# Kernel tuning notes

Hardware: AMD Instinct MI355X
Metric: run time of the kernel (lower is better)

Reference implementation:

```python
import jax, jax.numpy as jnp
import numpy as np

N_NODES = 100000
N_EDGES = 2000000
IN_X, IN_E, HID, OUT = 32, 64, 128, 64


def setup_inputs() -> dict:
    key = jax.random.key(0)
    ks = jax.random.split(key, 12)
    def w(k, shape, fan_in):
        return jax.random.normal(k, shape, dtype=jnp.float32) / np.sqrt(fan_in)
    x = jax.random.normal(ks[0], (N_NODES, IN_X), dtype=jnp.float32)
    edge_index = jax.random.randint(ks[1], (2, N_EDGES), 0, N_NODES)
    return {
        "x": x,
        "edge_index": edge_index,
        # initial_lin: in_x -> in_e
        "W0": w(ks[2], (IN_X, IN_E), IN_X),
        "b0": jnp.zeros((IN_E,), jnp.float32),
        # SAGEConv1: lin_l (aggregated neighbors, with bias), lin_r (self, no bias)
        "W1l": w(ks[3], (IN_E, HID), IN_E),
        "b1l": jnp.zeros((HID,), jnp.float32),
        "W1r": w(ks[4], (IN_E, HID), IN_E),
        # SAGEConv2
        "W2l": w(ks[5], (HID, OUT), HID),
        "b2l": jnp.zeros((OUT,), jnp.float32),
        "W2r": w(ks[6], (HID, OUT), HID),
        # pred head: 2*out -> 1
        "Wp": w(ks[7], (2 * OUT, 1), 2 * OUT),
        "bp": jnp.zeros((1,), jnp.float32),
    }


def _sage_conv(x, edge_index, Wl, bl, Wr):
    # PyG SAGEConv, aggr='mean': out = lin_l(mean_{j in N(i)} x_j) + lin_r(x_i)
    src, dst = edge_index[0], edge_index[1]
    n = x.shape[0]
    msg = x[src]                                   # [E, F] gather
    ssum = jax.ops.segment_sum(msg, dst, num_segments=n)          # [N, F]
    cnt = jax.ops.segment_sum(jnp.ones((edge_index.shape[1],), x.dtype), dst,
                              num_segments=n)                      # [N]
    aggr = ssum / jnp.maximum(cnt, 1.0)[:, None]
    return aggr @ Wl + bl + x @ Wr


def reference(x, edge_index, W0, b0, W1l, b1l, W1r, W2l, b2l, W2r, Wp, bp):
    h = x @ W0 + b0                                # initial_lin
    h = jax.nn.relu(_sage_conv(h, edge_index, W1l, b1l, W1r))
    # dropout p=0.5 is identity in eval mode
    h = _sage_conv(h, edge_index, W2l, b2l, W2r)   # [N, OUT]
    src, dst = edge_index[0], edge_index[1]
    combined = jnp.concatenate([h[src], h[dst]], axis=1)  # [E, 2*OUT]
    raw = (combined @ Wp + bp)[:, 0]               # squeeze -> [E]
    return raw, jax.nn.sigmoid(raw)
```

## Files before the change

kernel.cpp:

```cpp
#include <hip/hip_runtime.h>
#include <hip/hip_bf16.h>
#include <hip/hip_fp16.h>


#define IN_X 32
#define IN_E 64
#define HID 128
#define OUTF 64

#define BSHIFT 7
#define BSZ 128
#define NBP 1024
#define CHUNK 4096
#define CAP 4096

typedef _Float16 f16x8 __attribute__((ext_vector_type(8)));
typedef float f32x4 __attribute__((ext_vector_type(4)));

__device__ __forceinline__ float2 h2f2(uint v) {
  __half2 h = *reinterpret_cast<__half2*>(&v);
  return __half22float2(h);
}
__device__ __forceinline__ __half2 u2h(uint v) {
  return *reinterpret_cast<__half2*>(&v);
}
__device__ __forceinline__ uint h2u(__half2 h) {
  return *reinterpret_cast<uint*>(&h);
}

__global__ __launch_bounds__(256) void k_prep(
    const float* __restrict__ W0, const float* __restrict__ b0,
    const float* __restrict__ W1l, const float* __restrict__ b1l,
    const float* __restrict__ W1r,
    const float* __restrict__ W2l, const float* __restrict__ W2r,
    const float* __restrict__ b2l, const float* __restrict__ Wp,
    __half* __restrict__ U1T, __half* __restrict__ U2T, float* __restrict__ c1,
    float* __restrict__ svecs, float* __restrict__ hb, int* __restrict__ gcursor,
    const float* __restrict__ x, __half* __restrict__ xh, int xtotal) {
  const int blk = blockIdx.x;
  if (blk < 32) {
    __shared__ float sW0[IN_X * IN_E];
    for (int t = threadIdx.x; t < IN_X * IN_E; t += 256) sW0[t] = W0[t];
    __syncthreads();
    const int o = blk * 256 + threadIdx.x;
    const int hf = o >> 12;
    const int rem = o & 4095;
    const int j = rem >> 5, i = rem & 31;
    const float* W = hf ? W1r : W1l;
    float u = 0.f;
    #pragma unroll 8
    for (int k = 0; k < IN_E; ++k) u += sW0[i * IN_E + k] * W[k * HID + j];
    (hf ? U2T : U1T)[j * IN_X + i] = __float2half(u);
  } else if (blk == 32) {
    const int j = threadIdx.x;
    if (j < HID) {
      float cv = b1l[j];
      for (int k = 0; k < IN_E; ++k)
        cv += b0[k] * (W1l[k * HID + j] + W1r[k * HID + j]);
      c1[j] = cv;
    } else if (j == HID || j == HID + 1) {
      const float* w = Wp + (j - HID) * OUTF;
      float s = 0.f;
      for (int k = 0; k < OUTF; ++k) s += b2l[k] * w[k];
      hb[j - HID] = s;
    }
  } else if (blk == 33 || blk == 34) {
    __shared__ float sW[HID * OUTF];
    const float* W = (blk == 33) ? W2l : W2r;
    for (int t = threadIdx.x; t < HID * OUTF; t += 256) sW[t] = W[t];
    __syncthreads();
    const int vec = threadIdx.x >> 7;
    const int j = threadIdx.x & 127;
    const float* w = Wp + vec * OUTF;
    float s = 0.f;
    #pragma unroll 8
    for (int k = 0; k < OUTF; ++k) s += sW[j * OUTF + k] * w[k];
    svecs[(blk - 33) * 256 + vec * 128 + j] = s;
  } else if (blk == 35) {
    #pragma unroll
    for (int k = 0; k < NBP / 256; ++k) gcursor[k * 256 + threadIdx.x] = 0;
  } else {
    int i = ((blk - 36) * 256 + threadIdx.x) * 8;
    if (i < xtotal) {
      float4 a = *(const float4*)(x + i);
      float4 b = *(const float4*)(x + i + 4);
      __half2 h0 = __floats2half2_rn(a.x, a.y);
      __half2 h1 = __floats2half2_rn(a.z, a.w);
      __half2 h2 = __floats2half2_rn(b.x, b.y);
      __half2 h3 = __floats2half2_rn(b.z, b.w);
      uint4 o = { *(uint*)&h0, *(uint*)&h1, *(uint*)&h2, *(uint*)&h3 };
      *(uint4*)(xh + i) = o;
    }
  }
}

__global__ __launch_bounds__(512) void k_scatfuse(const int* __restrict__ src,
    const int* __restrict__ dst, int* __restrict__ gcursor,
    uint* __restrict__ bucketData, int E) {
  __shared__ int hist[NBP];
  const int cblk = blockIdx.x;
  for (int i = threadIdx.x; i < NBP; i += 512) hist[i] = 0;
  __syncthreads();
  const int base = cblk * CHUNK;
  int d[CHUNK / 512], s[CHUNK / 512];
  #pragma unroll
  for (int k = 0; k < CHUNK / 512; ++k) {
    int e = base + k * 512 + threadIdx.x;
    d[k] = (e < E) ? dst[e] : -1;
    s[k] = (e < E) ? src[e] : 0;
  }
  #pragma unroll
  for (int k = 0; k < CHUNK / 512; ++k)
    if (d[k] >= 0) atomicAdd(&hist[d[k] >> BSHIFT], 1);
  __syncthreads();
  for (int i = threadIdx.x; i < NBP; i += 512) {
    int h = hist[i];
    hist[i] = (h > 0) ? atomicAdd(&gcursor[i], h) : 0;
  }
  __syncthreads();
  #pragma unroll
  for (int k = 0; k < CHUNK / 512; ++k) {
    if (d[k] >= 0) {
      int bkt = d[k] >> BSHIFT;
      int pos = atomicAdd(&hist[bkt], 1);
      if (pos < CAP)
        bucketData[(size_t)bkt * CAP + pos] =
            ((uint)s[k] << BSHIFT) | (uint)(d[k] & (BSZ - 1));
    }
  }
}

__global__ __launch_bounds__(512) void k_baggr32s(const __half* __restrict__ feat,
    const uint* __restrict__ bucketData, const int* __restrict__ gcnt,
    __half* __restrict__ aggr, uint* __restrict__ gorder,
    int* __restrict__ gns, int* __restrict__ gne, int N, int Nhalf) {
  constexpr int FW = IN_X;
  __shared__ int nodeStart[2 * BSZ + 1];
  __shared__ int cursor[2 * BSZ];
  __shared__ int order[CAP];
  __shared__ uint2 stash[BSZ * 8];
  const int b = blockIdx.x;
  const int tid = threadIdx.x;
  const int lane = tid & 63, wid = tid >> 6;
  const int e0 = b * CAP;
  const int cnt = min(gcnt[b], CAP);

  for (int i = tid; i < 2 * BSZ; i += 512) cursor[i] = 0;
  __syncthreads();
  for (int i = tid; i < cnt; i += 512) {
    uint p = bucketData[e0 + i];
    int key = ((p & (BSZ - 1)) << 1) | ((int)(p >> BSHIFT) >= Nhalf ? 1 : 0);
    atomicAdd(&cursor[key], 1);
  }
  __syncthreads();

  if (wid == 0) {
    int carry = 0;
    #pragma unroll
    for (int seg = 0; seg < 4; ++seg) {
      int v = cursor[seg * 64 + lane];
      int x = v;
      #pragma unroll
      for (int s = 1; s < 64; s <<= 1) {
        int y = __shfl_up(x, s, 64);
        if (lane >= s) x += y;
      }
      nodeStart[seg * 64 + lane] = carry + x - v;
      carry += __shfl(x, 63, 64);
    }
    if (lane == 0) nodeStart[2 * BSZ] = carry;
  }
  __syncthreads();
  for (int i = tid; i < 2 * BSZ; i += 512) cursor[i] = nodeStart[i];
  __syncthreads();

  for (int i = tid; i < cnt; i += 512) {
    uint p = bucketData[e0 + i];
    int key = ((p & (BSZ - 1)) << 1) | ((int)(p >> BSHIFT) >= Nhalf ? 1 : 0);
    int pos = atomicAdd(&cursor[key], 1);
    order[pos] = (int)(p >> BSHIFT);
  }
  __syncthreads();

  for (int i = tid; i < cnt; i += 512) gorder[e0 + i] = (uint)order[i];
  if (tid < BSZ) {
    const int n = b * BSZ + tid;
    if (n < N) {
      gns[n] = e0 + nodeStart[2 * tid];
      gne[n] = e0 + nodeStart[2 * tid + 2];
    }
  }

  const int nodes = min(BSZ, N - b * BSZ);
  const int g = lane >> 3, e = lane & 7;

  for (int n = wid; n < nodes; n += 8) {
    const int s = nodeStart[2 * n], t = nodeStart[2 * n + 1];
    __half2 ax = __floats2half2_rn(0.f, 0.f), ay = ax;
    int j = s;
    for (; j + 16 <= t; j += 16) {
      int r0 = order[j + g], r1 = order[j + 8 + g];
      uint2 v0 = ((const uint2*)(feat + (size_t)r0 * FW))[e];
      uint2 v1 = ((const uint2*)(feat + (size_t)r1 * FW))[e];
      ax = __hadd2(ax, __hadd2(u2h(v0.x), u2h(v1.x)));
      ay = __hadd2(ay, __hadd2(u2h(v0.y), u2h(v1.y)));
    }
    for (; j < t; j += 8) {
      if (j + g < t) {
        int r = order[j + g];
        uint2 v = ((const uint2*)(feat + (size_t)r * FW))[e];
        ax = __hadd2(ax, u2h(v.x));
        ay = __hadd2(ay, u2h(v.y));
      }
    }
    #pragma unroll
    for (int m = 8; m < 64; m <<= 1) {
      ax = __hadd2(ax, u2h((uint)__shfl_xor((int)h2u(ax), m, 64)));
      ay = __hadd2(ay, u2h((uint)__shfl_xor((int)h2u(ay), m, 64)));
    }
    if (g == 0) stash[n * 8 + e] = make_uint2(h2u(ax), h2u(ay));
  }
  __syncthreads();

  for (int n = wid; n < nodes; n += 8) {
    const int s = nodeStart[2 * n + 1], t = nodeStart[2 * n + 2];
    __half2 ax = __floats2half2_rn(0.f, 0.f), ay = ax;
    int j = s;
    for (; j + 16 <= t; j += 16) {
      int r0 = order[j + g], r1 = order[j + 8 + g];
      uint2 v0 = ((const uint2*)(feat + (size_t)r0 * FW))[e];
      uint2 v1 = ((const uint2*)(feat + (size_t)r1 * FW))[e];
      ax = __hadd2(ax, __hadd2(u2h(v0.x), u2h(v1.x)));
      ay = __hadd2(ay, __hadd2(u2h(v0.y), u2h(v1.y)));
    }
    for (; j < t; j += 8) {
      if (j + g < t) {
        int r = order[j + g];
        uint2 v = ((const uint2*)(feat + (size_t)r * FW))[e];
        ax = __hadd2(ax, u2h(v.x));
        ay = __hadd2(ay, u2h(v.y));
      }
    }
    #pragma unroll
    for (int m = 8; m < 64; m <<= 1) {
      ax = __hadd2(ax, u2h((uint)__shfl_xor((int)h2u(ax), m, 64)));
      ay = __hadd2(ay, u2h((uint)__shfl_xor((int)h2u(ay), m, 64)));
    }
    if (g == 0) {
      uint2 st = stash[n * 8 + e];
      ax = __hadd2(ax, u2h(st.x));
      ay = __hadd2(ay, u2h(st.y));
      const int deg = nodeStart[2 * n + 2] - nodeStart[2 * n];
      float inv = 1.f / fmaxf((float)deg, 1.f);
      float2 fx = __half22float2(ax), fy = __half22float2(ay);
      __half2 o0 = __floats2half2_rn(fx.x * inv, fx.y * inv);
      __half2 o1 = __floats2half2_rn(fy.x * inv, fy.y * inv);
      uint2 o = { h2u(o0), h2u(o1) };
      ((uint2*)(aggr + ((size_t)(b * BSZ + n)) * FW))[e] = o;
    }
  }
}

__global__ __launch_bounds__(256) void k_conv1fused(
    const __half* __restrict__ axm, const __half* __restrict__ xh,
    const __half* __restrict__ U1T, const __half* __restrict__ U2T,
    const float* __restrict__ c1, const float* __restrict__ svecs,
    float2* __restrict__ tsd, float2* __restrict__ ssd, int N) {
  __shared__ _Float16 tile[4][16 * HID];
  __shared__ float svec[512];
  const int lane = threadIdx.x & 63;
  const int wid = threadIdx.x >> 6;
  const int row0 = blockIdx.x * 64 + wid * 16;
  const int lr = lane & 15;
  const int lk = (lane >> 4) * 8;

  for (int i = threadIdx.x; i < 512; i += 256) svec[i] = svecs[i];

  {
    f16x8 b1[8], b2[8];
    #pragma unroll
    for (int ct = 0; ct < 8; ++ct) {
      const int c = ct * 16 + lr;
      b1[ct] = *(const f16x8*)((const _Float16*)U1T + (size_t)c * IN_X + lk);
      b2[ct] = *(const f16x8*)((const _Float16*)U2T + (size_t)c * IN_X + lk);
    }
    f32x4 acc[8];
    #pragma unroll
    for (int ct = 0; ct < 8; ++ct) {
      float bv = c1[ct * 16 + lr];
      acc[ct] = (f32x4){bv, bv, bv, bv};
    }
    const int rA = min(row0 + lr, N - 1);
    f16x8 a1 = *(const f16x8*)((const _Float16*)axm + (size_t)rA * IN_X + lk);
    f16x8 a2 = *(const f16x8*)((const _Float16*)xh + (size_t)rA * IN_X + lk);
    #pragma unroll
    for (int ct = 0; ct < 8; ++ct)
      acc[ct] = __builtin_amdgcn_mfma_f32_16x16x32_f16(a1, b1[ct], acc[ct], 0, 0, 0);
    #pragma unroll
    for (int ct = 0; ct < 8; ++ct)
      acc[ct] = __builtin_amdgcn_mfma_f32_16x16x32_f16(a2, b2[ct], acc[ct], 0, 0, 0);
    #pragma unroll
    for (int ct = 0; ct < 8; ++ct) {
      #pragma unroll
      for (int r = 0; r < 4; ++r) {
        const int row = (lane >> 4) * 4 + r;
        const int col = ct * 16 + lr;
        int idx = (row * HID + col) ^ ((row & 7) << 3);
        tile[wid][idx] = (_Float16)fmaxf(acc[ct][r], 0.f);
      }
    }
  }
  __syncthreads();

  const int row = lane & 15, q = lane >> 4;
  float ts = 0.f, td = 0.f, ss = 0.f, sd = 0.f;
  #pragma unroll
  for (int t = 0; t < 4; ++t) {
    const int col = q * 32 + t * 8;
    int idx = (row * HID + col) ^ ((row & 7) << 3);
    f16x8 h = *(const f16x8*)&tile[wid][idx];
    #pragma unroll
    for (int i = 0; i < 8; ++i) {
      float hv = (float)h[i];
      ts += hv * svec[col + i];
      td += hv * svec[128 + col + i];
      ss += hv * svec[256 + col + i];
      sd += hv * svec[384 + col + i];
    }
  }
  ts += __shfl_xor(ts, 16, 64); ts += __shfl_xor(ts, 32, 64);
  td += __shfl_xor(td, 16, 64); td += __shfl_xor(td, 32, 64);
  ss += __shfl_xor(ss, 16, 64); ss += __shfl_xor(ss, 32, 64);
  sd += __shfl_xor(sd, 16, 64); sd += __shfl_xor(sd, 32, 64);
  if (q == 0) {
    const int grow = row0 + row;
    if (grow < N) {
      tsd[grow] = make_float2(ts, td);
      ssd[grow] = make_float2(ss, sd);
    }
  }
}

__global__ __launch_bounds__(256) void k_scalagg(const float2* __restrict__ tsd,
    const float2* __restrict__ ssd, const int* __restrict__ gns,
    const int* __restrict__ gne, const uint* __restrict__ gorder,
    const float* __restrict__ hb,
    float* __restrict__ gs, float* __restrict__ gd, int N) {
  const int n = blockIdx.x * 256 + threadIdx.x;
  if (n >= N) return;
  const int s = gns[n], t = gne[n];
  float ax = 0.f, ay = 0.f;
  int j = s;
  for (; j + 4 <= t; j += 4) {
    int r0 = (int)gorder[j],     r1 = (int)gorder[j + 1];
    int r2 = (int)gorder[j + 2], r3 = (int)gorder[j + 3];
    float2 a = tsd[r0], b = tsd[r1], c = tsd[r2], d = tsd[r3];
    ax += (a.x + b.x) + (c.x + d.x);
    ay += (a.y + b.y) + (c.y + d.y);
  }
  for (; j < t; ++j) {
    float2 a = tsd[(int)gorder[j]];
    ax += a.x; ay += a.y;
  }
  const float inv = 1.f / fmaxf((float)(t - s), 1.f);
  const float2 sv = ssd[n];
  gs[n] = sv.x + ax * inv + hb[0];
  gd[n] = sv.y + ay * inv + hb[1];
}

__global__ __launch_bounds__(256) void k_edge(const float* __restrict__ gs,
    const float* __restrict__ gd, const int* __restrict__ srcI,
    const int* __restrict__ dstI, const float* __restrict__ bp,
    float* __restrict__ out, int E) {
  int e = blockIdx.x * 256 + threadIdx.x;
  if (e >= E) return;
  float raw = gs[srcI[e]] + gd[dstI[e]] + bp[0];
  out[e] = raw;
  out[(size_t)E + e] = 1.f / (1.f + expf(-raw));
}

extern "C" void kernel_launch(void* const* d_in, const int* in_sizes, int n_in,
                              void* d_out, int out_size, void* d_ws, size_t ws_size,
                              hipStream_t stream) {
  const float* x   = (const float*)d_in[0];
  const int*   ei  = (const int*)d_in[1];
  const float* W0  = (const float*)d_in[2];
  const float* b0  = (const float*)d_in[3];
  const float* W1l = (const float*)d_in[4];
  const float* b1l = (const float*)d_in[5];
  const float* W1r = (const float*)d_in[6];
  const float* W2l = (const float*)d_in[7];
  const float* b2l = (const float*)d_in[8];
  const float* W2r = (const float*)d_in[9];
  const float* Wp  = (const float*)d_in[10];
  const float* bp  = (const float*)d_in[11];

  const int N = in_sizes[0] / IN_X;
  const int E = in_sizes[1] / 2;
  const int* srcI = ei;
  const int* dstI = ei + E;
  float* out = (float*)d_out;

  const int NB = (N + BSZ - 1) >> BSHIFT;
  const int nchunk = (E + CHUNK - 1) / CHUNK;

  __half* xh  = (__half*)d_ws;
  __half* axm = xh + (size_t)N * IN_X;
  float2* tsd = (float2*)(axm + (size_t)N * IN_X);
  float2* ssd = tsd + N;
  float* gs   = (float*)(ssd + N);
  float* gd   = gs + N;
  uintptr_t wp = ((uintptr_t)(gd + N) + 15) & ~(uintptr_t)15;
  __half* U1T  = (__half*)wp;
  __half* U2T  = U1T + HID * IN_X;
  float* c1    = (float*)(U2T + HID * IN_X);
  float* svecs = c1 + HID;
  float* hb    = svecs + 512;
  int* gcursor = (int*)(hb + 2);
  int* gns     = gcursor + NBP;
  int* gne     = gns + N + 1;
  uint* bucketData = (uint*)(gne + N);
  uint* gorder     = bucketData + (size_t)NBP * CAP;

  const int xblocks = (N * IN_X / 8 + 255) / 256;
  k_prep<<<36 + xblocks, 256, 0, stream>>>(W0, b0, W1l, b1l, W1r, W2l, W2r,
                                           b2l, Wp, U1T, U2T, c1, svecs, hb,
                                           gcursor, x, xh, N * IN_X);
  k_scatfuse<<<nchunk, 512, 0, stream>>>(srcI, dstI, gcursor, bucketData, E);
  k_baggr32s<<<NB, 512, 0, stream>>>(xh, bucketData, gcursor, axm, gorder,
                                     gns, gne, N, N / 2);
  k_conv1fused<<<(N + 63) / 64, 256, 0, stream>>>(axm, xh, U1T, U2T, c1,
                                                  svecs, tsd, ssd, N);
  k_scalagg<<<(N + 255) / 256, 256, 0, stream>>>(tsd, ssd, gns, gne, gorder,
                                                 hb, gs, gd, N);
  k_edge<<<(E + 255) / 256, 256, 0, stream>>>(gs, gd, srcI, dstI, bp, out, E);
}
```

Measured before the change: 128.9 us.

## Fuse first-layer aggregation with conv1 MFMA and projection into one kernel

```diff
diff --git a/kernel.cpp b/kernel.cpp
--- a/kernel.cpp
+++ b/kernel.cpp
@@ -130,21 +130,28 @@
   }
 }
 
-__global__ __launch_bounds__(512) void k_baggr32s(const __half* __restrict__ feat,
+__global__ __launch_bounds__(512) void k_baggrfuse(const __half* __restrict__ feat,
     const uint* __restrict__ bucketData, const int* __restrict__ gcnt,
-    __half* __restrict__ aggr, uint* __restrict__ gorder,
-    int* __restrict__ gns, int* __restrict__ gne, int N, int Nhalf) {
+    const __half* __restrict__ U1T, const __half* __restrict__ U2T,
+    const float* __restrict__ c1g, const float* __restrict__ svecs,
+    uint* __restrict__ gorder, int* __restrict__ gns, int* __restrict__ gne,
+    float2* __restrict__ tsd, float2* __restrict__ ssd, int N, int Nhalf) {
   constexpr int FW = IN_X;
   __shared__ int nodeStart[2 * BSZ + 1];
   __shared__ int cursor[2 * BSZ];
   __shared__ int order[CAP];
   __shared__ uint2 stash[BSZ * 8];
+  __shared__ _Float16 axmT[BSZ * FW];
+  __shared__ float svec[512];
+  __shared__ float c1s[HID];
   const int b = blockIdx.x;
   const int tid = threadIdx.x;
   const int lane = tid & 63, wid = tid >> 6;
   const int e0 = b * CAP;
   const int cnt = min(gcnt[b], CAP);
 
+  for (int i = tid; i < 512; i += 512) svec[i] = svecs[i];
+  if (tid < HID) c1s[tid] = c1g[tid];
   for (int i = tid; i < 2 * BSZ; i += 512) cursor[i] = 0;
   __syncthreads();
   for (int i = tid; i < cnt; i += 512) {
@@ -194,149 +201,106 @@
   const int nodes = min(BSZ, N - b * BSZ);
   const int g = lane >> 3, e = lane & 7;
 
-  for (int n = wid; n < nodes; n += 8) {
-    const int s = nodeStart[2 * n], t = nodeStart[2 * n + 1];
-    __half2 ax = __floats2half2_rn(0.f, 0.f), ay = ax;
-    int j = s;
-    for (; j + 16 <= t; j += 16) {
-      int r0 = order[j + g], r1 = order[j + 8 + g];
-      uint2 v0 = ((const uint2*)(feat + (size_t)r0 * FW))[e];
-      uint2 v1 = ((const uint2*)(feat + (size_t)r1 * FW))[e];
-      ax = __hadd2(ax, __hadd2(u2h(v0.x), u2h(v1.x)));
-      ay = __hadd2(ay, __hadd2(u2h(v0.y), u2h(v1.y)));
-    }
-    for (; j < t; j += 8) {
-      if (j + g < t) {
-        int r = order[j + g];
-        uint2 v = ((const uint2*)(feat + (size_t)r * FW))[e];
-        ax = __hadd2(ax, u2h(v.x));
-        ay = __hadd2(ay, u2h(v.y));
-      }
-    }
-    #pragma unroll
-    for (int m = 8; m < 64; m <<= 1) {
-      ax = __hadd2(ax, u2h((uint)__shfl_xor((int)h2u(ax), m, 64)));
-      ay = __hadd2(ay, u2h((uint)__shfl_xor((int)h2u(ay), m, 64)));
-    }
-    if (g == 0) stash[n * 8 + e] = make_uint2(h2u(ax), h2u(ay));
-  }
-  __syncthreads();
-
-  for (int n = wid; n < nodes; n += 8) {
-    const int s = nodeStart[2 * n + 1], t = nodeStart[2 * n + 2];
-    __half2 ax = __floats2half2_rn(0.f, 0.f), ay = ax;
-    int j = s;
-    for (; j + 16 <= t; j += 16) {
-      int r0 = order[j + g], r1 = order[j + 8 + g];
-      uint2 v0 = ((const uint2*)(feat + (size_t)r0 * FW))[e];
-      uint2 v1 = ((const uint2*)(feat + (size_t)r1 * FW))[e];
-      ax = __hadd2(ax, __hadd2(u2h(v0.x), u2h(v1.x)));
-      ay = __hadd2(ay, __hadd2(u2h(v0.y), u2h(v1.y)));
-    }
-    for (; j < t; j += 8) {
-      if (j + g < t) {
-        int r = order[j + g];
-        uint2 v = ((const uint2*)(feat + (size_t)r * FW))[e];
-        ax = __hadd2(ax, u2h(v.x));
-        ay = __hadd2(ay, u2h(v.y));
-      }
-    }
-    #pragma unroll
-    for (int m = 8; m < 64; m <<= 1) {
-      ax = __hadd2(ax, u2h((uint)__shfl_xor((int)h2u(ax), m, 64)));
-      ay = __hadd2(ay, u2h((uint)__shfl_xor((int)h2u(ay), m, 64)));
-    }
-    if (g == 0) {
-      uint2 st = stash[n * 8 + e];
-      ax = __hadd2(ax, u2h(st.x));
-      ay = __hadd2(ay, u2h(st.y));
-      const int deg = nodeStart[2 * n + 2] - nodeStart[2 * n];
-      float inv = 1.f / fmaxf((float)deg, 1.f);
-      float2 fx = __half22float2(ax), fy = __half22float2(ay);
-      __half2 o0 = __floats2half2_rn(fx.x * inv, fx.y * inv);
-      __half2 o1 = __floats2half2_rn(fy.x * inv, fy.y * inv);
-      uint2 o = { h2u(o0), h2u(o1) };
-      ((uint2*)(aggr + ((size_t)(b * BSZ + n)) * FW))[e] = o;
-    }
-  }
-}
-
-__global__ __launch_bounds__(256) void k_conv1fused(
-    const __half* __restrict__ axm, const __half* __restrict__ xh,
-    const __half* __restrict__ U1T, const __half* __restrict__ U2T,
-    const float* __restrict__ c1, const float* __restrict__ svecs,
-    float2* __restrict__ tsd, float2* __restrict__ ssd, int N) {
-  __shared__ _Float16 tile[4][16 * HID];
-  __shared__ float svec[512];
-  const int lane = threadIdx.x & 63;
-  const int wid = threadIdx.x >> 6;
-  const int row0 = blockIdx.x * 64 + wid * 16;
+  #pragma unroll
+  for (int ph = 0; ph < 2; ++ph) {
+    for (int n = wid; n < nodes; n += 8) {
+      const int s = nodeStart[2 * n + ph], t = nodeStart[2 * n + ph + 1];
+      __half2 ax = __floats2half2_rn(0.f, 0.f), ay = ax;
+      int j = s;
+      for (; j + 16 <= t; j += 16) {
+        int r0 = order[j + g], r1 = order[j + 8 + g];
+        uint2 v0 = ((const uint2*)(feat + (size_t)r0 * FW))[e];
+        uint2 v1 = ((const uint2*)(feat + (size_t)r1 * FW))[e];
+        ax = __hadd2(ax, __hadd2(u2h(v0.x), u2h(v1.x)));
+        ay = __hadd2(ay, __hadd2(u2h(v0.y), u2h(v1.y)));
+      }
+      for (; j < t; j += 8) {
+        if (j + g < t) {
+          int r = order[j + g];
+          uint2 v = ((const uint2*)(feat + (size_t)r * FW))[e];
+          ax = __hadd2(ax, u2h(v.x));
+          ay = __hadd2(ay, u2h(v.y));
+        }
+      }
+      #pragma unroll
+      for (int m = 8; m < 64; m <<= 1) {
+        ax = __hadd2(ax, u2h((uint)__shfl_xor((int)h2u(ax), m, 64)));
+        ay = __hadd2(ay, u2h((uint)__shfl_xor((int)h2u(ay), m, 64)));
+      }
+      if (g == 0) {
+        if (ph == 0) {
+          stash[n * 8 + e] = make_uint2(h2u(ax), h2u(ay));
+        } else {
+          uint2 st = stash[n * 8 + e];
+          ax = __hadd2(ax, u2h(st.x)); ay = __hadd2(ay, u2h(st.y));
+          const int deg = nodeStart[2 * n + 2] - nodeStart[2 * n];
+          float inv = 1.f / fmaxf((float)deg, 1.f);
+          float2 fx = __half22float2(ax), fy = __half22float2(ay);
+          __half2 o0 = __floats2half2_rn(fx.x * inv, fx.y * inv);
+          __half2 o1 = __floats2half2_rn(fy.x * inv, fy.y * inv);
+          ((uint2*)axmT)[n * 8 + e] = make_uint2(h2u(o0), h2u(o1));
+        }
+      }
+    }
+    __syncthreads();
+  }
+
   const int lr = lane & 15;
   const int lk = (lane >> 4) * 8;
-
-  for (int i = threadIdx.x; i < 512; i += 256) svec[i] = svecs[i];
-
-  {
-    f16x8 b1[8], b2[8];
+  const int rowbase = wid * 16;
+
+  f16x8 a1 = *(const f16x8*)&axmT[(rowbase + lr) * FW + lk];
+  const int rA = min(b * BSZ + rowbase + lr, N - 1);
+  f16x8 a2 = *(const f16x8*)((const _Float16*)feat + (size_t)rA * FW + lk);
+
+  f32x4 acc[8];
+  #pragma unroll
+  for (int ct = 0; ct < 8; ++ct) {
+    float bv = c1s[ct * 16 + lr];
+    acc[ct] = (f32x4){bv, bv, bv, bv};
+  }
+  #pragma unroll
+  for (int h = 0; h < 2; ++h) {
+    f16x8 b1[4], b2[4];
+    #pragma unroll
+    for (int q = 0; q < 4; ++q) {
+      const int c = (h * 4 + q) * 16 + lr;
+      b1[q] = *(const f16x8*)((const _Float16*)U1T + (size_t)c * IN_X + lk);
+      b2[q] = *(const f16x8*)((const _Float16*)U2T + (size_t)c * IN_X + lk);
+    }
+    #pragma unroll
+    for (int q = 0; q < 4; ++q)
+      acc[h * 4 + q] = __builtin_amdgcn_mfma_f32_16x16x32_f16(a1, b1[q], acc[h * 4 + q], 0, 0, 0);
+    #pragma unroll
+    for (int q = 0; q < 4; ++q)
+      acc[h * 4 + q] = __builtin_amdgcn_mfma_f32_16x16x32_f16(a2, b2[q], acc[h * 4 + q], 0, 0, 0);
+  }
+
+  #pragma unroll
+  for (int r = 0; r < 4; ++r) {
+    float ts = 0.f, td = 0.f, ss = 0.f, sd = 0.f;
     #pragma unroll
     for (int ct = 0; ct < 8; ++ct) {
-      const int c = ct * 16 + lr;
-      b1[ct] = *(const f16x8*)((const _Float16*)U1T + (size_t)c * IN_X + lk);
-      b2[ct] = *(const f16x8*)((const _Float16*)U2T + (size_t)c * IN_X + lk);
-    }
-    f32x4 acc[8];
-    #pragma unroll
-    for (int ct = 0; ct < 8; ++ct) {
-      float bv = c1[ct * 16 + lr];
-      acc[ct] = (f32x4){bv, bv, bv, bv};
-    }
-    const int rA = min(row0 + lr, N - 1);
-    f16x8 a1 = *(const f16x8*)((const _Float16*)axm + (size_t)rA * IN_X + lk);
-    f16x8 a2 = *(const f16x8*)((const _Float16*)xh + (size_t)rA * IN_X + lk);
-    #pragma unroll
-    for (int ct = 0; ct < 8; ++ct)
-      acc[ct] = __builtin_amdgcn_mfma_f32_16x16x32_f16(a1, b1[ct], acc[ct], 0, 0, 0);
-    #pragma unroll
-    for (int ct = 0; ct < 8; ++ct)
-      acc[ct] = __builtin_amdgcn_mfma_f32_16x16x32_f16(a2, b2[ct], acc[ct], 0, 0, 0);
-    #pragma unroll
-    for (int ct = 0; ct < 8; ++ct) {
-      #pragma unroll
-      for (int r = 0; r < 4; ++r) {
-        const int row = (lane >> 4) * 4 + r;
-        const int col = ct * 16 + lr;
-        int idx = (row * HID + col) ^ ((row & 7) << 3);
-        tile[wid][idx] = (_Float16)fmaxf(acc[ct][r], 0.f);
-      }
-    }
-  }
-  __syncthreads();
-
-  const int row = lane & 15, q = lane >> 4;
-  float ts = 0.f, td = 0.f, ss = 0.f, sd = 0.f;
-  #pragma unroll
-  for (int t = 0; t < 4; ++t) {
-    const int col = q * 32 + t * 8;
-    int idx = (row * HID + col) ^ ((row & 7) << 3);
-    f16x8 h = *(const f16x8*)&tile[wid][idx];
-    #pragma unroll
-    for (int i = 0; i < 8; ++i) {
-      float hv = (float)h[i];
-      ts += hv * svec[col + i];
-      td += hv * svec[128 + col + i];
-      ss += hv * svec[256 + col + i];
-      sd += hv * svec[384 + col + i];
-    }
-  }
-  ts += __shfl_xor(ts, 16, 64); ts += __shfl_xor(ts, 32, 64);
-  td += __shfl_xor(td, 16, 64); td += __shfl_xor(td, 32, 64);
-  ss += __shfl_xor(ss, 16, 64); ss += __shfl_xor(ss, 32, 64);
-  sd += __shfl_xor(sd, 16, 64); sd += __shfl_xor(sd, 32, 64);
-  if (q == 0) {
-    const int grow = row0 + row;
-    if (grow < N) {
-      tsd[grow] = make_float2(ts, td);
-      ssd[grow] = make_float2(ss, sd);
+      const float hv = fmaxf(acc[ct][r], 0.f);
+      const int col = ct * 16 + lr;
+      ts += hv * svec[col];
+      td += hv * svec[128 + col];
+      ss += hv * svec[256 + col];
+      sd += hv * svec[384 + col];
+    }
+    #pragma unroll
+    for (int m = 1; m < 16; m <<= 1) {
+      ts += __shfl_xor(ts, m, 64);
+      td += __shfl_xor(td, m, 64);
+      ss += __shfl_xor(ss, m, 64);
+      sd += __shfl_xor(sd, m, 64);
+    }
+    if (lr == 0) {
+      const int grow = b * BSZ + rowbase + (lane >> 4) * 4 + r;
+      if (grow < N) {
+        tsd[grow] = make_float2(ts, td);
+        ssd[grow] = make_float2(ss, sd);
+      }
     }
   }
 }
@@ -405,8 +369,7 @@
   const int nchunk = (E + CHUNK - 1) / CHUNK;
 
   __half* xh  = (__half*)d_ws;
-  __half* axm = xh + (size_t)N * IN_X;
-  float2* tsd = (float2*)(axm + (size_t)N * IN_X);
+  float2* tsd = (float2*)(xh + (size_t)N * IN_X);
   float2* ssd = tsd + N;
   float* gs   = (float*)(ssd + N);
   float* gd   = gs + N;
@@ -427,10 +390,9 @@
                                            b2l, Wp, U1T, U2T, c1, svecs, hb,
                                            gcursor, x, xh, N * IN_X);
   k_scatfuse<<<nchunk, 512, 0, stream>>>(srcI, dstI, gcursor, bucketData, E);
-  k_baggr32s<<<NB, 512, 0, stream>>>(xh, bucketData, gcursor, axm, gorder,
-                                     gns, gne, N, N / 2);
-  k_conv1fused<<<(N + 63) / 64, 256, 0, stream>>>(axm, xh, U1T, U2T, c1,
-                                                  svecs, tsd, ssd, N);
+  k_baggrfuse<<<NB, 512, 0, stream>>>(xh, bucketData, gcursor, U1T, U2T, c1,
+                                      svecs, gorder, gns, gne, tsd, ssd,
+                                      N, N / 2);
   k_scalagg<<<(N + 255) / 256, 256, 0, stream>>>(tsd, ssd, gns, gne, gorder,
                                                  hb, gs, gd, N);
   k_edge<<<(E + 255) / 256, 256, 0, stream>>>(gs, gd, srcI, dstI, bp, out, E);
```

Result: slower. 151.2 us (+17.3%).
